# Performance work log

Hardware: AMD Instinct MI355X
Metric: run time of the kernel (lower is better)

## Reference

```python
import jax, jax.numpy as jnp
import numpy as np

B, S, H = 2, 2048, 768
NH, DH = 12, 64  # num_heads, dim_head; inner_dim = NH*DH = H
SCALE = DH ** -0.5


def setup_inputs() -> dict:
    key = jax.random.key(0)
    k1, k2, k3 = jax.random.split(key, 3)
    x = jax.random.normal(k1, (B, S, H), dtype=jnp.float32)
    w_qkv = jax.random.normal(k2, (3 * NH * DH, H), dtype=jnp.float32) * (H ** -0.5)
    w_out = jax.random.normal(k3, (H, NH * DH), dtype=jnp.float32) * ((NH * DH) ** -0.5)
    b_out = jnp.zeros((H,), dtype=jnp.float32)
    return {"x": x, "w_qkv": w_qkv, "w_out": w_out, "b_out": b_out}


def reference(x, w_qkv, w_out, b_out):
    b, s, _ = x.shape
    # qkv linear: [b, s, 3*inner]
    qkv = jnp.einsum('bsh,oh->bso', x, w_qkv)
    # 'b s (qkv l d) -> qkv b l s d'  (l = heads)
    qkv = qkv.reshape(b, s, 3, NH, DH).transpose(2, 0, 3, 1, 4)
    q, k, v = qkv[0], qkv[1], qkv[2]  # each [b, nh, s, dh]
    att = jax.nn.softmax(jnp.einsum('bhxd,bhyd->bhxy', q, k) * SCALE, axis=-1)
    out = jnp.einsum('bhxy,bhyd->bhxd', att, v)  # [b, nh, s, dh]
    out = out.transpose(0, 2, 1, 3).reshape(b, s, NH * DH)  # 'b h l d -> b l (h d)'
    return jnp.einsum('bsi,oi->bso', out, w_out) + b_out
```

## Files before the change

kernel.cpp:

```cpp
#include <hip/hip_runtime.h>
#include <cstdint>
#include <cstddef>

typedef __bf16 bf16;
typedef __bf16 bf16x8 __attribute__((ext_vector_type(8)));
typedef __bf16 bf16x4 __attribute__((ext_vector_type(4)));
typedef float  f32x4  __attribute__((ext_vector_type(4)));
typedef float  f32x16 __attribute__((ext_vector_type(16)));

constexpr int Bb  = 2;
constexpr int Ss  = 2048;
constexpr int Hh  = 768;
constexpr int NHh = 12;
constexpr int DHh = 64;
constexpr int Mm  = Bb * Ss;
constexpr int N3  = 3 * Hh;
constexpr int QKW = 2 * Hh;

__device__ __forceinline__ float fexp2(float x) { return __builtin_amdgcn_exp2f(x); }

__device__ __forceinline__ void gload_lds16(void* lds, const void* g) {
  __builtin_amdgcn_global_load_lds(
      (__attribute__((address_space(1))) void*)(uintptr_t)g,
      (__attribute__((address_space(3))) void*)(uint32_t)(uintptr_t)lds,
      16, 0, 0);
}

__global__ void cvt3_f32_bf16(const float* __restrict__ x,  bf16* __restrict__ xb,
                              const float* __restrict__ w1, bf16* __restrict__ w1b,
                              const float* __restrict__ w2, bf16* __restrict__ w2b) {
  const int st = gridDim.x * blockDim.x;
  int i0 = blockIdx.x * blockDim.x + threadIdx.x;
  for (int i = i0; i < 786432; i += st) {
    float4 v = ((const float4*)x)[i];
    bf16x4 o; o[0]=(bf16)v.x; o[1]=(bf16)v.y; o[2]=(bf16)v.z; o[3]=(bf16)v.w;
    ((bf16x4*)xb)[i] = o;
  }
  for (int i = i0; i < 442368; i += st) {
    float4 v = ((const float4*)w1)[i];
    bf16x4 o; o[0]=(bf16)v.x; o[1]=(bf16)v.y; o[2]=(bf16)v.z; o[3]=(bf16)v.w;
    ((bf16x4*)w1b)[i] = o;
  }
  for (int i = i0; i < 147456; i += st) {
    float4 v = ((const float4*)w2)[i];
    bf16x4 o; o[0]=(bf16)v.x; o[1]=(bf16)v.y; o[2]=(bf16)v.z; o[3]=(bf16)v.w;
    ((bf16x4*)w2b)[i] = o;
  }
}

template<int OUTMODE, int BM>
__global__ __launch_bounds__(256, 2)
void gemm_bt(const bf16* __restrict__ A, const bf16* __restrict__ Bw,
             bf16* __restrict__ Qb, bf16* __restrict__ Kf, bf16* __restrict__ Vf,
             float* __restrict__ Cf, const float* __restrict__ bias)
{
  constexpr int K = 768;
  constexpr int NT = K / 32;
  constexpr int MI = BM / 32;
  constexpr int ABUF = BM * 64;
  __shared__ bf16 As[2][BM * 32];
  __shared__ bf16 Bs[2][128 * 32];
  const int tid  = threadIdx.x;
  const int wid  = tid >> 6, lane = tid & 63;
  const int lr   = lane & 15, lk = lane >> 4;
  const int n0   = blockIdx.x * 128, m0 = blockIdx.y * BM;
  const int wm   = (wid >> 1) * (BM / 2), wn = (wid & 1) * 64;

  f32x4 acc[MI][4] = {};

  const char* Ag = (const char*)(A  + (size_t)m0 * K) + (size_t)(tid >> 2) * (K * 2) + (tid & 3) * 16;
  const char* Bg = (const char*)(Bw + (size_t)n0 * K) + (size_t)(tid >> 2) * (K * 2) + (tid & 3) * 16;
  constexpr size_t rstep = (size_t)64 * K * 2;

  auto stage = [&](int buf, int kb) {
    char* aw = (char*)As + buf * ABUF + wid * 1024;
    char* bw = (char*)Bs + buf * 8192 + wid * 1024;
    gload_lds16(aw, Ag + (size_t)kb * 2);
    if constexpr (BM == 128)
      gload_lds16(aw + 4096, Ag + rstep + (size_t)kb * 2);
    gload_lds16(bw,        Bg + (size_t)kb * 2);
    gload_lds16(bw + 4096, Bg + rstep + (size_t)kb * 2);
  };

  stage(0, 0);
  asm volatile("s_waitcnt vmcnt(0)" ::: "memory");
  __syncthreads();

#pragma unroll 1
  for (int t = 0; t < NT; ++t) {
    const int cur = t & 1;
    if (t + 1 < NT) stage(cur ^ 1, (t + 1) * 32);
    __builtin_amdgcn_sched_barrier(0);

    bf16x8 af[MI], bfv[4];
#pragma unroll
    for (int i = 0; i < MI; ++i)
      af[i]  = *(const bf16x8*)((const char*)As + cur * ABUF + ((wm + i * 16 + lr) * 32 + lk * 8) * 2);
#pragma unroll
    for (int j = 0; j < 4; ++j)
      bfv[j] = *(const bf16x8*)((const char*)Bs + cur * 8192 + ((wn + j * 16 + lr) * 32 + lk * 8) * 2);
#pragma unroll
    for (int i = 0; i < MI; ++i)
#pragma unroll
      for (int j = 0; j < 4; ++j)
        acc[i][j] = __builtin_amdgcn_mfma_f32_16x16x32_bf16(af[i], bfv[j], acc[i][j], 0, 0, 0);

    __syncthreads();
  }

  if constexpr (OUTMODE == 1) {
#pragma unroll
    for (int i = 0; i < MI; ++i)
#pragma unroll
      for (int j = 0; j < 4; ++j) {
        const int n = n0 + wn + j * 16 + lr;
        const float bv = bias[n];
#pragma unroll
        for (int r = 0; r < 4; ++r) {
          const int m = m0 + wm + i * 16 + lk * 4 + r;
          Cf[(size_t)m * Hh + n] = acc[i][j][r] + bv;
        }
      }
  } else {
    const int bidx = m0 >> 11;
    const int kvb  = (m0 & 2047) + wm + lk * 4;
    if (n0 < Hh) {
#pragma unroll
      for (int i = 0; i < MI; ++i)
#pragma unroll
        for (int j = 0; j < 4; ++j) {
          const int n = n0 + wn + j * 16 + lr;
#pragma unroll
          for (int r = 0; r < 4; ++r) {
            const int m = m0 + wm + i * 16 + lk * 4 + r;
            Qb[(size_t)m * Hh + n] = (bf16)acc[i][j][r];
          }
        }
    } else if (n0 < QKW) {
#pragma unroll
      for (int i = 0; i < MI; ++i)
#pragma unroll
        for (int j = 0; j < 4; ++j) {
          const int colv = (n0 - Hh) + wn + j * 16 + lr;
          const int hh = colv >> 6, dd = colv & 63;
          bf16* kfh = Kf + (size_t)(bidx * NHh + hh) * 131072;
#pragma unroll
          for (int r = 0; r < 4; ++r) {
            const int kv = kvb + i * 16 + r;
            const size_t idx = (size_t)((((kv >> 5) * 4 + (dd >> 4)) * 64
                                + ((dd >> 3) & 1) * 32 + (kv & 31)) * 8 + (dd & 7));
            kfh[idx] = (bf16)acc[i][j][r];
          }
        }
    } else {
#pragma unroll
      for (int i = 0; i < MI; ++i)
#pragma unroll
        for (int j = 0; j < 4; ++j) {
          const int colv = (n0 - QKW) + wn + j * 16 + lr;
          const int hh = colv >> 6, dd = colv & 63;
          const int bh = bidx * NHh + hh;
          const int mb = kvb + i * 16;
          bf16x4 pv;
#pragma unroll
          for (int r = 0; r < 4; ++r) pv[r] = (bf16)acc[i][j][r];
          const size_t idx8 = (((size_t)bh * 128 + (mb >> 4)) * 2 + (dd >> 5)) * 64
                              + ((mb >> 3) & 1) * 32 + (dd & 31);
          *(bf16x4*)(Vf + idx8 * 8 + (mb & 7)) = pv;
        }
    }
  }
}

__global__ __launch_bounds__(256, 3)
void attn_fwd7(const bf16* __restrict__ Qb, const bf16* __restrict__ Kfrag,
               const bf16* __restrict__ Vfrag, bf16* __restrict__ aout)
{
  __shared__ __align__(16) char lds[17408];
  const int tid  = threadIdx.x;
  const int wid  = tid >> 6, lane = tid & 63;
  const int lq   = lane & 31, hi = lane >> 5;
  const int qh   = wid & 1, grp = wid >> 1;

  const int orig = blockIdx.x;
  const int swz  = (orig & 7) * 96 + (orig >> 3);
  const int qb   = swz & 31;
  const int bh   = swz >> 5;
  const int b    = bh / NHh, h = bh % NHh;
  const int q0   = qb * 64 + qh * 32;

  constexpr float Cs = 0.18033688011112042f;
  const bf16* qrow = Qb + (size_t)(b * Ss + q0 + lq) * Hh + h * DHh;
  bf16x8 qf[4];
#pragma unroll
  for (int j = 0; j < 4; ++j) {
    bf16x8 t = *(const bf16x8*)(qrow + j * 16 + hi * 8);
#pragma unroll
    for (int e = 0; e < 8; ++e) t[e] = (bf16)((float)t[e] * Cs);
    qf[j] = t;
  }

  const char* Kfp = (const char*)Kfrag + (size_t)bh * 262144 + grp * 131072 + lane * 16;
  const char* Vfp = (const char*)Vfrag + (size_t)bh * 262144 + grp * 131072 + lane * 16;

  f32x16 oacc[2] = {};
  float rsum = 0.f;
  bf16x8 kfA[2][4], kfB[2][4], vf[4][2];

#pragma unroll
  for (int kvc = 0; kvc < 2; ++kvc)
#pragma unroll
    for (int j = 0; j < 4; ++j)
      kfA[kvc][j] = *(const bf16x8*)(Kfp + kvc * 4096 + j * 1024);
#pragma unroll
  for (int s4 = 0; s4 < 4; ++s4)
#pragma unroll
    for (int dc = 0; dc < 2; ++dc)
      vf[s4][dc] = *(const bf16x8*)(Vfp + (s4 * 2 + dc) * 1024);

  auto step = [&](bf16x8 (&KC)[2][4], bf16x8 (&KN)[2][4], int i) {
    f32x16 s0 = {};
    __builtin_amdgcn_s_setprio(1);
#pragma unroll
    for (int j = 0; j < 4; ++j)
      s0 = __builtin_amdgcn_mfma_f32_32x32x16_bf16(KC[0][j], qf[j], s0, 0, 0, 0);
    __builtin_amdgcn_s_setprio(0);

    uint32_t w0[8];
    float rp0 = 0.f, rp1 = 0.f;
#pragma unroll
    for (int m = 0; m < 8; ++m) {
      const float e0 = fexp2(s0[2 * m]);
      const float e1 = fexp2(s0[2 * m + 1]);
      rp0 += e0; rp1 += e1;
      union { bf16 hh[2]; uint32_t u; } cv;
      cv.hh[0] = (bf16)e0; cv.hh[1] = (bf16)e1;
      w0[m] = cv.u;
    }

    f32x16 s1 = {};
    __builtin_amdgcn_s_setprio(1);
#pragma unroll
    for (int j = 0; j < 4; ++j)
      s1 = __builtin_amdgcn_mfma_f32_32x32x16_bf16(KC[1][j], qf[j], s1, 0, 0, 0);
    __builtin_amdgcn_s_setprio(0);

    __builtin_amdgcn_sched_barrier(0);
    {
      const char* kp = Kfp + (size_t)(((i + 1) & 15) * 8192);
#pragma unroll
      for (int kvc = 0; kvc < 2; ++kvc)
#pragma unroll
        for (int j = 0; j < 4; ++j)
          KN[kvc][j] = *(const bf16x8*)(kp + kvc * 4096 + j * 1024);
    }
    __builtin_amdgcn_sched_barrier(0);

    uint32_t w1[8];
#pragma unroll
    for (int m = 0; m < 8; ++m) {
      const float e0 = fexp2(s1[2 * m]);
      const float e1 = fexp2(s1[2 * m + 1]);
      rp0 += e0; rp1 += e1;
      union { bf16 hh[2]; uint32_t u; } cv;
      cv.hh[0] = (bf16)e0; cv.hh[1] = (bf16)e1;
      w1[m] = cv.u;
    }
    rsum += rp0 + rp1;

    __builtin_amdgcn_s_setprio(1);
#pragma unroll
    for (int s4 = 0; s4 < 4; ++s4) {
      const int sb = s4 & 1;
      const uint32_t* wp = (s4 < 2) ? w0 : w1;
      uint32_t a0 = wp[4 * sb + 0], b0 = wp[4 * sb + 2];
      uint32_t a1 = wp[4 * sb + 1], b1 = wp[4 * sb + 3];
      asm("v_permlane32_swap_b32 %0, %1" : "+v"(a0), "+v"(b0));
      asm("v_permlane32_swap_b32 %0, %1" : "+v"(a1), "+v"(b1));
      union { uint32_t u[4]; bf16x8 v; } pf;
      pf.u[0] = a0; pf.u[1] = a1; pf.u[2] = b0; pf.u[3] = b1;
#pragma unroll
      for (int dc = 0; dc < 2; ++dc)
        oacc[dc] = __builtin_amdgcn_mfma_f32_32x32x16_bf16(vf[s4][dc], pf.v, oacc[dc], 0, 0, 0);
    }
    __builtin_amdgcn_s_setprio(0);

    __builtin_amdgcn_sched_barrier(0);
    {
      const char* vp = Vfp + (size_t)(((i + 1) & 15) * 8192);
#pragma unroll
      for (int s4 = 0; s4 < 4; ++s4)
#pragma unroll
        for (int dc = 0; dc < 2; ++dc)
          vf[s4][dc] = *(const bf16x8*)(vp + (s4 * 2 + dc) * 1024);
    }
    __builtin_amdgcn_sched_barrier(0);
  };

#pragma unroll 1
  for (int ii = 0; ii < 8; ++ii) {
    step(kfA, kfB, 2 * ii);
    step(kfB, kfA, 2 * ii + 1);
  }

  rsum += __shfl_xor(rsum, 32, 64);

  __syncthreads();

  if (grp == 1) {
    char* mb = lds + qh * 8704;
#pragma unroll
    for (int dc = 0; dc < 2; ++dc)
#pragma unroll
      for (int rr = 0; rr < 4; ++rr) {
        f32x4 t;
#pragma unroll
        for (int e = 0; e < 4; ++e) t[e] = oacc[dc][rr * 4 + e];
        *(f32x4*)(mb + (dc * 4 + rr) * 1024 + lane * 16) = t;
      }
    *(float*)(mb + 8192 + lane * 4) = rsum;
  }
  __syncthreads();
  if (grp == 0) {
    const char* mb = lds + qh * 8704;
    const float l2 = *(const float*)(mb + 8192 + lane * 4);
    const float linv = 1.0f / (rsum + l2);
    bf16* orow = aout + (size_t)(b * Ss + q0 + lq) * Hh + h * DHh;
#pragma unroll
    for (int dc = 0; dc < 2; ++dc)
#pragma unroll
      for (int rr = 0; rr < 4; ++rr) {
        const f32x4 o2 = *(const f32x4*)(mb + (dc * 4 + rr) * 1024 + lane * 16);
        bf16x4 ov;
#pragma unroll
        for (int e = 0; e < 4; ++e)
          ov[e] = (bf16)((oacc[dc][rr * 4 + e] + o2[e]) * linv);
        *(bf16x4*)(orow + dc * 32 + rr * 8 + hi * 4) = ov;
      }
  }
}

extern "C" void kernel_launch(void* const* d_in, const int* in_sizes, int n_in,
                              void* d_out, int out_size, void* d_ws, size_t ws_size,
                              hipStream_t stream) {
  const float* x     = (const float*)d_in[0];
  const float* w_qkv = (const float*)d_in[1];
  const float* w_out = (const float*)d_in[2];
  const float* b_out = (const float*)d_in[3];
  char* ws = (char*)d_ws;
  bf16* xb    = (bf16*)(ws + 0);
  bf16* wqkvb = (bf16*)(ws + 6291456);
  bf16* woutb = (bf16*)(ws + 9830400);
  bf16* Qb    = (bf16*)(ws + 11010048);
  bf16* Kfrag = (bf16*)(ws + 17301504);
  bf16* Vfrag = (bf16*)(ws + 23592960);
  bf16* aoutb = (bf16*)(ws + 29884416);

  cvt3_f32_bf16<<<2048, 256, 0, stream>>>(x, xb, w_qkv, wqkvb, w_out, woutb);

  gemm_bt<0, 128><<<dim3(18, 32), 256, 0, stream>>>(xb, wqkvb, Qb, Kfrag, Vfrag,
                                                    nullptr, nullptr);
  attn_fwd7<<<768, 256, 0, stream>>>(Qb, Kfrag, Vfrag, aoutb);
  gemm_bt<1, 64><<<dim3(6, 64), 256, 0, stream>>>(aoutb, woutb, nullptr, nullptr, nullptr,
                                                  (float*)d_out, b_out);
}
```

Measured before the change: 105.2 us.

## Split attention KV across four waves per 32-query tile and swizzle GEMM blocks

The attention kernel now gives each block one 32-query tile and splits the key/value sequence four ways across its waves, where before it used two query halves and a two-way KV split. This doubles the grid to 1536 blocks, and wave 0 reduces three partial outputs through a transposed LDS layout. The GEMMs switch to a 1D grid with an XCD-aware block swizzle, and their launch bounds rise from 2 to 3 blocks per SIMD. The change aims at better occupancy and latency hiding in attention and better L2 locality in the GEMMs, at the cost of a larger LDS reduction and more register pressure from the higher launch bound.

After: 107.7 us. 1.02x slower.

```diff
diff --git a/kernel.cpp b/kernel.cpp
--- a/kernel.cpp
+++ b/kernel.cpp
@@ -25,6 +25,8 @@
       (__attribute__((address_space(3))) void*)(uint32_t)(uintptr_t)lds,
       16, 0, 0);
 }
+
+__device__ __forceinline__ void cfence() { asm volatile("" ::: "memory"); }
 
 __global__ void cvt3_f32_bf16(const float* __restrict__ x,  bf16* __restrict__ xb,
                               const float* __restrict__ w1, bf16* __restrict__ w1b,
@@ -48,8 +50,8 @@
   }
 }
 
-template<int OUTMODE, int BM>
-__global__ __launch_bounds__(256, 2)
+template<int OUTMODE, int BM, int NXT>
+__global__ __launch_bounds__(256, 3)
 void gemm_bt(const bf16* __restrict__ A, const bf16* __restrict__ Bw,
              bf16* __restrict__ Qb, bf16* __restrict__ Kf, bf16* __restrict__ Vf,
              float* __restrict__ Cf, const float* __restrict__ bias)
@@ -63,7 +65,11 @@
   const int tid  = threadIdx.x;
   const int wid  = tid >> 6, lane = tid & 63;
   const int lr   = lane & 15, lk = lane >> 4;
-  const int n0   = blockIdx.x * 128, m0 = blockIdx.y * BM;
+
+  const int id   = blockIdx.x;
+  const int swz  = (id & 7) * (gridDim.x >> 3) + (id >> 3);
+  const int n0   = (swz % NXT) * 128;
+  const int m0   = (swz / NXT) * BM;
   const int wm   = (wid >> 1) * (BM / 2), wn = (wid & 1) * 64;
 
   f32x4 acc[MI][4] = {};
@@ -173,21 +179,20 @@
 }
 
 __global__ __launch_bounds__(256, 3)
-void attn_fwd7(const bf16* __restrict__ Qb, const bf16* __restrict__ Kfrag,
-               const bf16* __restrict__ Vfrag, bf16* __restrict__ aout)
+void attn_fwd12(const bf16* __restrict__ Qb, const bf16* __restrict__ Kfrag,
+                const bf16* __restrict__ Vfrag, bf16* __restrict__ aout)
 {
-  __shared__ __align__(16) char lds[17408];
+  __shared__ __align__(16) char lds[25088];
   const int tid  = threadIdx.x;
-  const int wid  = tid >> 6, lane = tid & 63;
+  const int grp  = tid >> 6, lane = tid & 63;
   const int lq   = lane & 31, hi = lane >> 5;
-  const int qh   = wid & 1, grp = wid >> 1;
 
   const int orig = blockIdx.x;
-  const int swz  = (orig & 7) * 96 + (orig >> 3);
-  const int qb   = swz & 31;
-  const int bh   = swz >> 5;
+  const int swz  = (orig & 7) * 192 + (orig >> 3);
+  const int qt   = swz & 63;
+  const int bh   = swz >> 6;
   const int b    = bh / NHh, h = bh % NHh;
-  const int q0   = qb * 64 + qh * 32;
+  const int q0   = qt * 32;
 
   constexpr float Cs = 0.18033688011112042f;
   const bf16* qrow = Qb + (size_t)(b * Ss + q0 + lq) * Hh + h * DHh;
@@ -200,8 +205,8 @@
     qf[j] = t;
   }
 
-  const char* Kfp = (const char*)Kfrag + (size_t)bh * 262144 + grp * 131072 + lane * 16;
-  const char* Vfp = (const char*)Vfrag + (size_t)bh * 262144 + grp * 131072 + lane * 16;
+  const char* Kfp = (const char*)Kfrag + (size_t)bh * 262144 + grp * 65536 + lane * 16;
+  const char* Vfp = (const char*)Vfrag + (size_t)bh * 262144 + grp * 65536 + lane * 16;
 
   f32x16 oacc[2] = {};
   float rsum = 0.f;
@@ -247,7 +252,7 @@
 
     __builtin_amdgcn_sched_barrier(0);
     {
-      const char* kp = Kfp + (size_t)(((i + 1) & 15) * 8192);
+      const char* kp = Kfp + (size_t)(((i + 1) & 7) * 8192);
 #pragma unroll
       for (int kvc = 0; kvc < 2; ++kvc)
 #pragma unroll
@@ -287,7 +292,7 @@
 
     __builtin_amdgcn_sched_barrier(0);
     {
-      const char* vp = Vfp + (size_t)(((i + 1) & 15) * 8192);
+      const char* vp = Vfp + (size_t)(((i + 1) & 7) * 8192);
 #pragma unroll
       for (int s4 = 0; s4 < 4; ++s4)
 #pragma unroll
@@ -298,17 +303,15 @@
   };
 
 #pragma unroll 1
-  for (int ii = 0; ii < 8; ++ii) {
+  for (int ii = 0; ii < 4; ++ii) {
     step(kfA, kfB, 2 * ii);
     step(kfB, kfA, 2 * ii + 1);
   }
 
   rsum += __shfl_xor(rsum, 32, 64);
 
-  __syncthreads();
-
-  if (grp == 1) {
-    char* mb = lds + qh * 8704;
+  if (grp != 0) {
+    char* mb = lds + (grp - 1) * 8320;
 #pragma unroll
     for (int dc = 0; dc < 2; ++dc)
 #pragma unroll
@@ -316,25 +319,36 @@
         f32x4 t;
 #pragma unroll
         for (int e = 0; e < 4; ++e) t[e] = oacc[dc][rr * 4 + e];
-        *(f32x4*)(mb + (dc * 4 + rr) * 1024 + lane * 16) = t;
+        *(f32x4*)(mb + lane * 128 + (dc * 4 + rr) * 16) = t;
       }
-    *(float*)(mb + 8192 + lane * 4) = rsum;
+    if (lane < 32) *(float*)(mb + 8192 + lane * 4) = rsum;
   }
   __syncthreads();
   if (grp == 0) {
-    const char* mb = lds + qh * 8704;
-    const float l2 = *(const float*)(mb + 8192 + lane * 4);
-    const float linv = 1.0f / (rsum + l2);
+    float lt = rsum;
+#pragma unroll
+    for (int g = 0; g < 3; ++g) {
+      const char* mb = lds + g * 8320;
+      lt += *(const float*)(mb + 8192 + lq * 4);
+#pragma unroll
+      for (int dc = 0; dc < 2; ++dc)
+#pragma unroll
+        for (int rr = 0; rr < 4; ++rr) {
+          const f32x4 o2 = *(const f32x4*)(mb + lane * 128 + (dc * 4 + rr) * 16);
+#pragma unroll
+          for (int e = 0; e < 4; ++e) oacc[dc][rr * 4 + e] += o2[e];
+        }
+    }
+    const float linv = 1.0f / lt;
     bf16* orow = aout + (size_t)(b * Ss + q0 + lq) * Hh + h * DHh;
 #pragma unroll
     for (int dc = 0; dc < 2; ++dc)
 #pragma unroll
       for (int rr = 0; rr < 4; ++rr) {
-        const f32x4 o2 = *(const f32x4*)(mb + (dc * 4 + rr) * 1024 + lane * 16);
         bf16x4 ov;
 #pragma unroll
         for (int e = 0; e < 4; ++e)
-          ov[e] = (bf16)((oacc[dc][rr * 4 + e] + o2[e]) * linv);
+          ov[e] = (bf16)(oacc[dc][rr * 4 + e] * linv);
         *(bf16x4*)(orow + dc * 32 + rr * 8 + hi * 4) = ov;
       }
   }
@@ -358,9 +372,9 @@
 
   cvt3_f32_bf16<<<2048, 256, 0, stream>>>(x, xb, w_qkv, wqkvb, w_out, woutb);
 
-  gemm_bt<0, 128><<<dim3(18, 32), 256, 0, stream>>>(xb, wqkvb, Qb, Kfrag, Vfrag,
-                                                    nullptr, nullptr);
-  attn_fwd7<<<768, 256, 0, stream>>>(Qb, Kfrag, Vfrag, aoutb);
-  gemm_bt<1, 64><<<dim3(6, 64), 256, 0, stream>>>(aoutb, woutb, nullptr, nullptr, nullptr,
-                                                  (float*)d_out, b_out);
-}
+  gemm_bt<0, 128, 18><<<576, 256, 0, stream>>>(xb, wqkvb, Qb, Kfrag, Vfrag,
+                                               nullptr, nullptr);
+  attn_fwd12<<<1536, 256, 0, stream>>>(Qb, Kfrag, Vfrag, aoutb);
+  gemm_bt<1, 64, 6><<<384, 256, 0, stream>>>(aoutb, woutb, nullptr, nullptr, nullptr,
+                                             (float*)d_out, b_out);
+}
```
